# Performance work log

Hardware: AMD Instinct MI355X
Metric: run time of the kernel (lower is better)

## Reference

```python
import jax, jax.numpy as jnp
import numpy as np

CLIP = 50.0
EPS = 1e-8


def _attn_jacobian_agg(q, k, v, scale):
    """Aggregate attention Jacobian dO/dq summed over queries, plus attention outputs.

    q: (B, Q, d); k, v: (B, S, d).
    Per-query Jacobian: J_q = scale * sum_j p_j v_j (k_j - kbar)^T, kbar = sum_i p_i k_i.
    Returns (agg_jac: (B, d, d), outputs: (B, Q, d)).
    """
    scores = jnp.einsum('bqd,bsd->bqs', q, k) * scale
    p = jax.nn.softmax(scores, axis=-1)
    out = jnp.einsum('bqs,bsd->bqd', p, v)           # attention outputs O
    kbar = jnp.einsum('bqs,bsd->bqd', p, k)          # expected key per query
    # sum_j p_j v_j k_j^T  -> (B, Q, d, d)
    pvk = jnp.einsum('bqs,bsd,bse->bqde', p, v, k)
    jac = scale * (pvk - out[..., :, None] * kbar[..., None, :])
    return jac.sum(axis=1), out


def setup_inputs() -> dict:
    key = jax.random.key(0)
    ks = jax.random.split(key, 5)
    B, Q, S, M, D = 256, 16, 512, 8, 128
    return {
        'queries': jax.random.normal(ks[0], (B, Q, D), dtype=jnp.float32),
        'keys':    jax.random.normal(ks[1], (B, S, D), dtype=jnp.float32),
        'values':  jax.random.normal(ks[2], (B, S, D), dtype=jnp.float32),
        'k_cg':    jax.random.normal(ks[3], (B, M, D), dtype=jnp.float32),
        'v_cg':    jax.random.normal(ks[4], (B, M, D), dtype=jnp.float32),
    }


def reference(queries, keys, values, k_cg, v_cg):
    B, Q, d = queries.shape
    scale = d ** -0.5

    dense_jac, dense_out = _attn_jacobian_agg(queries, keys, values, scale)
    cg_jac, cg_out = _attn_jacobian_agg(queries, k_cg, v_cg, scale)

    # jacobian_clip_value = 50.0 (config default)
    dense_jac = jnp.clip(dense_jac, -CLIP, CLIP)
    cg_jac = jnp.clip(cg_jac, -CLIP, CLIP)

    df = dense_jac.reshape(B, -1)
    cf = cg_jac.reshape(B, -1)
    dn = jnp.linalg.norm(df, axis=-1)
    cn = jnp.linalg.norm(cf, axis=-1)
    cosine_sim = (df * cf).sum(axis=-1) / (dn * cn + EPS)
    force_direction_loss = 1.0 - cosine_sim

    # consistency: per-query output MSE, averaged over queries, scaled by 1/d_head
    out_diff = dense_out - cg_out
    per_query_mse = (out_diff ** 2).sum(axis=-1)          # (B, Q)
    consistency_loss = per_query_mse.sum(axis=-1) / Q / d  # (B,)

    # v4 loss: L = w_dir * L_force_cos + w_cons * L_consistency (defaults 1.0, 1.0)
    total = 1.0 * force_direction_loss + 1.0 * consistency_loss
    return total.mean()  # reduction='mean'
```

## Files before the change

### kernel.cpp

```cpp
#include <hip/hip_runtime.h>
#include <math.h>


namespace {
constexpr int Bn = 256, Qn = 16, Sn = 512, Mn = 8, Dn = 128;
constexpr int NT = 512;
constexpr float SCALE = 0.08838834764831845f;
constexpr float CLIPV = 50.0f;

constexpr int QS    = 0;
constexpr int PB    = 4352;
constexpr int WOFF  = 20992;
constexpr int ARENA = 23040;
constexpr int KT    = ARENA;
constexpr int VT    = ARENA + 18432;
constexpr int VTW   = ARENA + 27648;
constexpr int SCF   = ARENA;
constexpr int CGS   = 59904;
constexpr int PCG   = 60416;
constexpr int WC    = 61696;
constexpr int RED   = 61728;
constexpr int LDSZ  = 61856;

typedef __attribute__((ext_vector_type(8))) short bf16x8;
typedef __attribute__((ext_vector_type(4))) float f32x4;
#define MFMA16(a, b, c) __builtin_amdgcn_mfma_f32_16x16x32_bf16((a), (b), (c), 0, 0, 0)

__device__ inline unsigned int pack2t(float a, float b) {
  return __builtin_amdgcn_perm(__builtin_bit_cast(unsigned int, b),
                               __builtin_bit_cast(unsigned int, a), 0x07060302u);
}
__device__ inline unsigned short f2bf(float x) {
  unsigned int u = __builtin_bit_cast(unsigned int, x);
  u += 0x7fffu + ((u >> 16) & 1u);
  return (unsigned short)(u >> 16);
}
__device__ inline float bf2f(unsigned short h) {
  unsigned int u = ((unsigned int)h) << 16;
  return __builtin_bit_cast(float, u);
}
union Frag {
  bf16x8 v;
  unsigned int u[4];
  unsigned short h[8];
};

__global__ void zero_ws_kernel(float4* ws) {
  ws[threadIdx.x] = make_float4(0.f, 0.f, 0.f, 0.f);
}

__global__ void finalize_kernel(const float* __restrict__ ws, float* __restrict__ out) {
  __shared__ float sr[256];
  int i = threadIdx.x;
  float dt = ws[i * 4 + 0], n1 = ws[i * 4 + 1], n2 = ws[i * 4 + 2], cs = ws[i * 4 + 3];
  float cosv = dt / (sqrtf(n1) * sqrtf(n2) + 1e-8f);
  sr[i] = (1.0f - cosv) + cs * (1.0f / (float)(Qn * Dn));
  __syncthreads();
  for (int off = 128; off; off >>= 1) {
    if (i < off) sr[i] += sr[i + off];
    __syncthreads();
  }
  if (i == 0) out[0] = sr[0] * (1.0f / (float)Bn);
}

__global__ __launch_bounds__(NT, 4) void fm_kernel(
    const float* __restrict__ Qg, const float* __restrict__ Kg,
    const float* __restrict__ Vg, const float* __restrict__ Kcg,
    const float* __restrict__ Vcg, float* __restrict__ ws) {
  __shared__ __align__(16) char L[LDSZ];
  const int bid = blockIdx.x, b = bid >> 1, h = bid & 1;
  const int t = threadIdx.x, lane = t & 63, wv = t >> 6;
  const int quad = lane >> 4, l16 = lane & 15;

  const float* Qb = Qg + (size_t)b * Qn * Dn;
  const float* Kb = Kg + (size_t)b * Sn * Dn;
  const float* Vb = Vg + (size_t)b * Sn * Dn;
  const float* Kc = Kcg + (size_t)b * Mn * Dn;
  const float* Vc = Vcg + (size_t)b * Mn * Dn;

  const int dK = t & 127, gK = t >> 7;
  const int dV = t & 63, gV = t >> 6;
  float kpf[2][8], vpf[8];

  auto load_tiles = [&](int st) {
#pragma unroll
    for (int o = 0; o < 2; ++o) {
      int s0 = st * 64 + (gK + 4 * o) * 8;
#pragma unroll
      for (int i = 0; i < 8; ++i) kpf[o][i] = Kb[(size_t)(s0 + i) * Dn + dK];
    }
    int s1 = st * 64 + gV * 8;
#pragma unroll
    for (int i = 0; i < 8; ++i) vpf[i] = Vb[(size_t)(s1 + i) * Dn + h * 64 + dV];
  };
  auto store_tiles = [&](int st) {
#pragma unroll
    for (int o = 0; o < 2; ++o) {
      unsigned int u0 = pack2t(kpf[o][0], kpf[o][1]), u1 = pack2t(kpf[o][2], kpf[o][3]);
      unsigned int u2 = pack2t(kpf[o][4], kpf[o][5]), u3 = pack2t(kpf[o][6], kpf[o][7]);
      *(uint4*)(L + KT + dK * 144 + (gK + 4 * o) * 16) = make_uint4(u0, u1, u2, u3);
    }
    int s1 = st * 64 + gV * 8;
    float wv8[8];
#pragma unroll
    for (int i = 0; i < 8; ++i) wv8[i] = *(const float*)(L + WOFF + (s1 + i) * 4);
    unsigned int v0 = pack2t(vpf[0], vpf[1]), v1 = pack2t(vpf[2], vpf[3]);
    unsigned int v2 = pack2t(vpf[4], vpf[5]), v3 = pack2t(vpf[6], vpf[7]);
    *(uint4*)(L + VT + dV * 144 + gV * 16) = make_uint4(v0, v1, v2, v3);
    unsigned int w0 = pack2t(wv8[0] * vpf[0], wv8[1] * vpf[1]);
    unsigned int w1 = pack2t(wv8[2] * vpf[2], wv8[3] * vpf[3]);
    unsigned int w2 = pack2t(wv8[4] * vpf[4], wv8[5] * vpf[5]);
    unsigned int w3 = pack2t(wv8[6] * vpf[6], wv8[7] * vpf[7]);
    *(uint4*)(L + VTW + dV * 144 + gV * 16) = make_uint4(w0, w1, w2, w3);
  };

  {
    int row = t >> 5, c4 = t & 31;
    float4 qv = ((const float4*)Qb)[t];
    unsigned int p0 = pack2t(qv.x * SCALE, qv.y * SCALE);
    unsigned int p1 = pack2t(qv.z * SCALE, qv.w * SCALE);
    *(unsigned long long*)(L + QS + row * 272 + c4 * 8) =
        (unsigned long long)p0 | ((unsigned long long)p1 << 32);
  }
  load_tiles(0);
  __syncthreads();

  {
    bf16x8 aq[4];
#pragma unroll
    for (int kk = 0; kk < 4; ++kk)
      aq[kk] = *(const bf16x8*)(L + QS + l16 * 272 + kk * 64 + quad * 16);
    for (int j = 0; j < 4; ++j) {
      int srow = 64 * wv + 16 * j + l16;
      const float* kp = Kb + (size_t)srow * Dn + quad * 8;
      f32x4 acc = {0.f, 0.f, 0.f, 0.f};
#pragma unroll
      for (int kk = 0; kk < 4; ++kk) {
        float4 lo = *(const float4*)(kp + kk * 32);
        float4 hi = *(const float4*)(kp + kk * 32 + 4);
        Frag f;
        f.u[0] = pack2t(lo.x, lo.y);
        f.u[1] = pack2t(lo.z, lo.w);
        f.u[2] = pack2t(hi.x, hi.y);
        f.u[3] = pack2t(hi.z, hi.w);
        acc = MFMA16(aq[kk], f.v, acc);
      }
      int s = 64 * wv + 16 * j + l16;
#pragma unroll
      for (int r = 0; r < 4; ++r)
        *(float*)(L + SCF + (quad * 4 + r) * 2064 + s * 4) = acc[r];
    }
  }
  __syncthreads();

#pragma unroll
  for (int rr = 0; rr < 2; ++rr) {
    int q = wv * 2 + rr;
    const float* srow = (const float*)(L + SCF + q * 2064);
    float x[8];
    float m = -1e30f;
#pragma unroll
    for (int i = 0; i < 8; ++i) { x[i] = srow[lane * 8 + i]; m = fmaxf(m, x[i]); }
#pragma unroll
    for (int o = 32; o; o >>= 1) m = fmaxf(m, __shfl_xor(m, o));
    float ssum = 0.f;
#pragma unroll
    for (int i = 0; i < 8; ++i) { x[i] = __expf(x[i] - m); ssum += x[i]; }
#pragma unroll
    for (int o = 32; o; o >>= 1) ssum += __shfl_xor(ssum, o);
    float inv = 1.f / ssum;
    Frag g;
#pragma unroll
    for (int i = 0; i < 8; ++i) g.h[i] = f2bf(x[i] * inv);
    *(bf16x8*)(L + PB + q * 1040 + lane * 16) = g.v;
  }
  __syncthreads();
  {
    float wsv = 0.f;
#pragma unroll
    for (int q = 0; q < Qn; ++q)
      wsv += bf2f(*(const unsigned short*)(L + PB + q * 1040 + t * 2));
    *(float*)(L + WOFF + t * 4) = wsv;
  }
  __syncthreads();

  const int rp = wv & 1, ch = wv >> 1;
  f32x4 C00 = {0.f,0.f,0.f,0.f}, C01 = {0.f,0.f,0.f,0.f};
  f32x4 C10 = {0.f,0.f,0.f,0.f}, C11 = {0.f,0.f,0.f,0.f};
  f32x4 outacc = {0.f,0.f,0.f,0.f}, kbacc = {0.f,0.f,0.f,0.f};

  auto ckstep = [&](int colByte, f32x4& c00, f32x4& c01, f32x4& c10, f32x4& c11) {
    bf16x8 A0 = *(const bf16x8*)(L + VTW + (rp * 32 + l16) * 144 + colByte + quad * 16);
    bf16x8 A1 = *(const bf16x8*)(L + VTW + (rp * 32 + 16 + l16) * 144 + colByte + quad * 16);
    bf16x8 B0 = *(const bf16x8*)(L + KT + (ch * 32 + l16) * 144 + colByte + quad * 16);
    bf16x8 B1 = *(const bf16x8*)(L + KT + (ch * 32 + 16 + l16) * 144 + colByte + quad * 16);
    c00 = MFMA16(A0, B0, c00);
    c01 = MFMA16(A0, B1, c01);
    c10 = MFMA16(A1, B0, c10);
    c11 = MFMA16(A1, B1, c11);
  };

  for (int st = 0; st < 8; ++st) {
    if (st) __syncthreads();
    store_tiles(st);
    __syncthreads();
    if (st < 7) load_tiles(st + 1);
#pragma unroll
    for (int z = 0; z < 2; ++z) {
      int colByte = z * 64;
      bf16x8 pA = *(const bf16x8*)(L + PB + l16 * 1040 + st * 128 + z * 64 + quad * 16);
      bf16x8 bK = *(const bf16x8*)(L + KT + (wv * 16 + l16) * 144 + colByte + quad * 16);
      kbacc = MFMA16(pA, bK, kbacc);
      if (wv < 4) {
        bf16x8 bV = *(const bf16x8*)(L + VT + (wv * 16 + l16) * 144 + colByte + quad * 16);
        outacc = MFMA16(pA, bV, outacc);
      }
      ckstep(colByte, C00, C01, C10, C11);
    }
  }
  __syncthreads();

  if (wv < 4) {
#pragma unroll
    for (int r = 0; r < 4; ++r)
      *(unsigned short*)(L + VTW + (wv * 16 + l16) * 144 + (quad * 4 + r) * 2) = f2bf(-outacc[r]);
  }
#pragma unroll
  for (int r = 0; r < 4; ++r)
    *(unsigned short*)(L + KT + (wv * 16 + l16) * 144 + (quad * 4 + r) * 2) = f2bf(kbacc[r]);
  if (t < 256) {
    *(uint4*)(L + KT + (t >> 1) * 144 + 32 + (t & 1) * 16) = make_uint4(0, 0, 0, 0);
  } else if (t < 384) {
    int i = t - 256;
    *(uint4*)(L + VTW + (i >> 1) * 144 + 32 + (i & 1) * 16) = make_uint4(0, 0, 0, 0);
  }
  __syncthreads();
  ckstep(0, C00, C01, C10, C11);
#pragma unroll
  for (int r = 0; r < 4; ++r) {
    C00[r] = fminf(fmaxf(SCALE * C00[r], -CLIPV), CLIPV);
    C01[r] = fminf(fmaxf(SCALE * C01[r], -CLIPV), CLIPV);
    C10[r] = fminf(fmaxf(SCALE * C10[r], -CLIPV), CLIPV);
    C11[r] = fminf(fmaxf(SCALE * C11[r], -CLIPV), CLIPV);
  }
  __syncthreads();

  if (wv == 0) {
    f32x4 acc = {0.f, 0.f, 0.f, 0.f};
    const float* kp = Kc + (size_t)(l16 & 7) * Dn + quad * 8;
#pragma unroll
    for (int kk = 0; kk < 4; ++kk) {
      bf16x8 a = *(const bf16x8*)(L + QS + l16 * 272 + kk * 64 + quad * 16);
      float4 lo = *(const float4*)(kp + kk * 32);
      float4 hi = *(const float4*)(kp + kk * 32 + 4);
      Frag f;
      f.u[0] = pack2t(lo.x, lo.y);
      f.u[1] = pack2t(lo.z, lo.w);
      f.u[2] = pack2t(hi.x, hi.y);
      f.u[3] = pack2t(hi.z, hi.w);
      acc = MFMA16(a, f.v, acc);
    }
    if (l16 < 8) {
#pragma unroll
      for (int r = 0; r < 4; ++r)
        *(float*)(L + CGS + (quad * 4 + r) * 32 + l16 * 4) = acc[r];
    }
  }
  __syncthreads();
  if (t < 16) {
    float xs[8];
    float m = -1e30f;
#pragma unroll
    for (int s = 0; s < 8; ++s) { xs[s] = *(const float*)(L + CGS + t * 32 + s * 4); m = fmaxf(m, xs[s]); }
    float ssum = 0.f;
#pragma unroll
    for (int s = 0; s < 8; ++s) { xs[s] = __expf(xs[s] - m); ssum += xs[s]; }
    float inv = 1.f / ssum;
#pragma unroll
    for (int s = 0; s < 4; ++s)
      *(unsigned int*)(L + PCG + t * 80 + s * 4) = pack2t(xs[2 * s] * inv, xs[2 * s + 1] * inv);
#pragma unroll
    for (int p = 4; p < 16; ++p) *(unsigned int*)(L + PCG + t * 80 + p * 4) = 0u;
  }
  __syncthreads();
  if (t < 8) {
    float s = 0.f;
#pragma unroll
    for (int q = 0; q < Qn; ++q) s += bf2f(*(const unsigned short*)(L + PCG + q * 80 + t * 2));
    *(float*)(L + WC + t * 4) = s;
  }
  __syncthreads();
  if (t < 128) {
    float kv[8];
#pragma unroll
    for (int i = 0; i < 8; ++i) kv[i] = Kc[(size_t)i * Dn + t];
    *(uint4*)(L + KT + t * 144) = make_uint4(pack2t(kv[0], kv[1]), pack2t(kv[2], kv[3]),
                                             pack2t(kv[4], kv[5]), pack2t(kv[6], kv[7]));
    *(uint4*)(L + KT + t * 144 + 16) = make_uint4(0, 0, 0, 0);
    *(uint4*)(L + KT + t * 144 + 32) = make_uint4(0, 0, 0, 0);
    *(uint4*)(L + KT + t * 144 + 48) = make_uint4(0, 0, 0, 0);
  } else if (t < 192) {
    int d = t - 128;
    float vv2[8];
#pragma unroll
    for (int i = 0; i < 8; ++i) vv2[i] = Vc[(size_t)i * Dn + h * 64 + d];
    *(uint4*)(L + VT + d * 144) = make_uint4(pack2t(vv2[0], vv2[1]), pack2t(vv2[2], vv2[3]),
                                             pack2t(vv2[4], vv2[5]), pack2t(vv2[6], vv2[7]));
    *(uint4*)(L + VT + d * 144 + 16) = make_uint4(0, 0, 0, 0);
    *(uint4*)(L + VT + d * 144 + 32) = make_uint4(0, 0, 0, 0);
    *(uint4*)(L + VT + d * 144 + 48) = make_uint4(0, 0, 0, 0);
  } else if (t < 256) {
    int d = t - 192;
    float vv2[8], wcv[8];
#pragma unroll
    for (int i = 0; i < 8; ++i) {
      vv2[i] = Vc[(size_t)i * Dn + h * 64 + d];
      wcv[i] = *(const float*)(L + WC + i * 4);
    }
    *(uint4*)(L + VTW + d * 144) =
        make_uint4(pack2t(wcv[0] * vv2[0], wcv[1] * vv2[1]), pack2t(wcv[2] * vv2[2], wcv[3] * vv2[3]),
                   pack2t(wcv[4] * vv2[4], wcv[5] * vv2[5]), pack2t(wcv[6] * vv2[6], wcv[7] * vv2[7]));
    *(uint4*)(L + VTW + d * 144 + 16) = make_uint4(0, 0, 0, 0);
    *(uint4*)(L + VTW + d * 144 + 32) = make_uint4(0, 0, 0, 0);
    *(uint4*)(L + VTW + d * 144 + 48) = make_uint4(0, 0, 0, 0);
  }
  __syncthreads();
  f32x4 outc = {0.f,0.f,0.f,0.f}, kbc = {0.f,0.f,0.f,0.f};
  f32x4 D00 = {0.f,0.f,0.f,0.f}, D01 = {0.f,0.f,0.f,0.f};
  f32x4 D10 = {0.f,0.f,0.f,0.f}, D11 = {0.f,0.f,0.f,0.f};
  {
    bf16x8 pA = *(const bf16x8*)(L + PCG + l16 * 80 + quad * 16);
    bf16x8 bK = *(const bf16x8*)(L + KT + (wv * 16 + l16) * 144 + quad * 16);
    kbc = MFMA16(pA, bK, kbc);
    if (wv < 4) {
      bf16x8 bV = *(const bf16x8*)(L + VT + (wv * 16 + l16) * 144 + quad * 16);
      outc = MFMA16(pA, bV, outc);
    }
    ckstep(0, D00, D01, D10, D11);
  }
  __syncthreads();
  if (wv < 4) {
#pragma unroll
    for (int r = 0; r < 4; ++r)
      *(unsigned short*)(L + VTW + (wv * 16 + l16) * 144 + (quad * 4 + r) * 2) = f2bf(-outc[r]);
  }
#pragma unroll
  for (int r = 0; r < 4; ++r)
    *(unsigned short*)(L + KT + (wv * 16 + l16) * 144 + (quad * 4 + r) * 2) = f2bf(kbc[r]);
  __syncthreads();
  ckstep(0, D00, D01, D10, D11);
#pragma unroll
  for (int r = 0; r < 4; ++r) {
    D00[r] = fminf(fmaxf(SCALE * D00[r], -CLIPV), CLIPV);
    D01[r] = fminf(fmaxf(SCALE * D01[r], -CLIPV), CLIPV);
    D10[r] = fminf(fmaxf(SCALE * D10[r], -CLIPV), CLIPV);
    D11[r] = fminf(fmaxf(SCALE * D11[r], -CLIPV), CLIPV);
  }

  float dot = 0.f, nd2 = 0.f, nc2 = 0.f, cons = 0.f;
#pragma unroll
  for (int r = 0; r < 4; ++r) {
    dot += C00[r] * D00[r] + C01[r] * D01[r] + C10[r] * D10[r] + C11[r] * D11[r];
    nd2 += C00[r] * C00[r] + C01[r] * C01[r] + C10[r] * C10[r] + C11[r] * C11[r];
    nc2 += D00[r] * D00[r] + D01[r] * D01[r] + D10[r] * D10[r] + D11[r] * D11[r];
  }
  if (wv < 4) {
#pragma unroll
    for (int r = 0; r < 4; ++r) {
      float df = outacc[r] - outc[r];
      cons += df * df;
    }
  }
#pragma unroll
  for (int o = 32; o; o >>= 1) {
    dot += __shfl_xor(dot, o);
    nd2 += __shfl_xor(nd2, o);
    nc2 += __shfl_xor(nc2, o);
    cons += __shfl_xor(cons, o);
  }
  if (lane == 0) {
    float* red = (float*)(L + RED);
    red[wv * 4 + 0] = dot;
    red[wv * 4 + 1] = nd2;
    red[wv * 4 + 2] = nc2;
    red[wv * 4 + 3] = cons;
  }
  __syncthreads();
  if (t == 0) {
    const float* red = (const float*)(L + RED);
    float d_ = 0.f, n1 = 0.f, n2 = 0.f, cs = 0.f;
#pragma unroll
    for (int w = 0; w < 8; ++w) {
      d_ += red[w * 4 + 0];
      n1 += red[w * 4 + 1];
      n2 += red[w * 4 + 2];
      cs += red[w * 4 + 3];
    }
    atomicAdd(ws + b * 4 + 0, d_);
    atomicAdd(ws + b * 4 + 1, n1);
    atomicAdd(ws + b * 4 + 2, n2);
    atomicAdd(ws + b * 4 + 3, cs);
  }
}
}

extern "C" void kernel_launch(void* const* d_in, const int* in_sizes, int n_in,
                              void* d_out, int out_size, void* d_ws, size_t ws_size,
                              hipStream_t stream) {
  const float* q = (const float*)d_in[0];
  const float* k = (const float*)d_in[1];
  const float* v = (const float*)d_in[2];
  const float* kc = (const float*)d_in[3];
  const float* vc = (const float*)d_in[4];
  float* out = (float*)d_out;
  float* ws = (float*)d_ws;
  zero_ws_kernel<<<1, 256, 0, stream>>>((float4*)ws);
  fm_kernel<<<2 * Bn, NT, 0, stream>>>(q, k, v, kc, vc, ws);
  finalize_kernel<<<1, 256, 0, stream>>>(ws, out);
}
```

Measured before the change: 169.0 us.

## Double-buffer K/V register prefetch two stages ahead and prefetch cg tensors early

The K/V register prefetch becomes two buffers that load tiles two stages ahead, so global loads overlap more compute, and the first extra tile load is issued before the softmax. The small cg K/V loads are hoisted into stage 6 of the main loop to hide their latency. Blocks are remapped so the two halves of a batch sit 256 blocks apart, and the weight reads in store_tiles are vectorised into float4 loads. The extra register buffers raise VGPR pressure, which could hurt occupancy under launch_bounds(512,4) or cause spills.

```diff
diff --git a/kernel.cpp b/kernel.cpp
--- a/kernel.cpp
+++ b/kernel.cpp
@@ -68,7 +68,7 @@
     const float* __restrict__ Vg, const float* __restrict__ Kcg,
     const float* __restrict__ Vcg, float* __restrict__ ws) {
   __shared__ __align__(16) char L[LDSZ];
-  const int bid = blockIdx.x, b = bid >> 1, h = bid & 1;
+  const int bid = blockIdx.x, b = bid & 255, h = bid >> 8;
   const int t = threadIdx.x, lane = t & 63, wv = t >> 6;
   const int quad = lane >> 4, l16 = lane & 15;
 
@@ -80,9 +80,11 @@
 
   const int dK = t & 127, gK = t >> 7;
   const int dV = t & 63, gV = t >> 6;
-  float kpf[2][8], vpf[8];
-
-  auto load_tiles = [&](int st) {
+  float kpfA[2][8], vpfA[8];
+  float kpfB[2][8], vpfB[8];
+  float cgkv[8];
+
+  auto load_tiles = [&](int st, float (&kpf)[2][8], float (&vpf)[8]) {
 #pragma unroll
     for (int o = 0; o < 2; ++o) {
       int s0 = st * 64 + (gK + 4 * o) * 8;
@@ -93,7 +95,7 @@
 #pragma unroll
     for (int i = 0; i < 8; ++i) vpf[i] = Vb[(size_t)(s1 + i) * Dn + h * 64 + dV];
   };
-  auto store_tiles = [&](int st) {
+  auto store_tiles = [&](int st, float (&kpf)[2][8], float (&vpf)[8]) {
 #pragma unroll
     for (int o = 0; o < 2; ++o) {
       unsigned int u0 = pack2t(kpf[o][0], kpf[o][1]), u1 = pack2t(kpf[o][2], kpf[o][3]);
@@ -101,9 +103,9 @@
       *(uint4*)(L + KT + dK * 144 + (gK + 4 * o) * 16) = make_uint4(u0, u1, u2, u3);
     }
     int s1 = st * 64 + gV * 8;
-    float wv8[8];
-#pragma unroll
-    for (int i = 0; i < 8; ++i) wv8[i] = *(const float*)(L + WOFF + (s1 + i) * 4);
+    float4 wlo = *(const float4*)(L + WOFF + s1 * 4);
+    float4 whi = *(const float4*)(L + WOFF + s1 * 4 + 16);
+    float wv8[8] = {wlo.x, wlo.y, wlo.z, wlo.w, whi.x, whi.y, whi.z, whi.w};
     unsigned int v0 = pack2t(vpf[0], vpf[1]), v1 = pack2t(vpf[2], vpf[3]);
     unsigned int v2 = pack2t(vpf[4], vpf[5]), v3 = pack2t(vpf[6], vpf[7]);
     *(uint4*)(L + VT + dV * 144 + gV * 16) = make_uint4(v0, v1, v2, v3);
@@ -122,7 +124,7 @@
     *(unsigned long long*)(L + QS + row * 272 + c4 * 8) =
         (unsigned long long)p0 | ((unsigned long long)p1 << 32);
   }
-  load_tiles(0);
+  load_tiles(0, kpfA, vpfA);
   __syncthreads();
 
   {
@@ -151,6 +153,7 @@
         *(float*)(L + SCF + (quad * 4 + r) * 2064 + s * 4) = acc[r];
     }
   }
+  load_tiles(1, kpfB, vpfB);
   __syncthreads();
 
 #pragma unroll
@@ -200,11 +203,25 @@
     c11 = MFMA16(A1, B1, c11);
   };
 
+#pragma unroll 2
   for (int st = 0; st < 8; ++st) {
     if (st) __syncthreads();
-    store_tiles(st);
+    if (st & 1) store_tiles(st, kpfB, vpfB);
+    else       store_tiles(st, kpfA, vpfA);
     __syncthreads();
-    if (st < 7) load_tiles(st + 1);
+    if (st < 6) {
+      if (st & 1) load_tiles(st + 2, kpfB, vpfB);
+      else        load_tiles(st + 2, kpfA, vpfA);
+    } else if (st == 6) {
+      if (t < 128) {
+#pragma unroll
+        for (int i = 0; i < 8; ++i) cgkv[i] = Kc[(size_t)i * Dn + t];
+      } else if (t < 256) {
+        int d = (t - 128) & 63;
+#pragma unroll
+        for (int i = 0; i < 8; ++i) cgkv[i] = Vc[(size_t)i * Dn + h * 64 + d];
+      }
+    }
 #pragma unroll
     for (int z = 0; z < 2; ++z) {
       int colByte = z * 64;
@@ -291,35 +308,26 @@
   }
   __syncthreads();
   if (t < 128) {
-    float kv[8];
-#pragma unroll
-    for (int i = 0; i < 8; ++i) kv[i] = Kc[(size_t)i * Dn + t];
-    *(uint4*)(L + KT + t * 144) = make_uint4(pack2t(kv[0], kv[1]), pack2t(kv[2], kv[3]),
-                                             pack2t(kv[4], kv[5]), pack2t(kv[6], kv[7]));
+    *(uint4*)(L + KT + t * 144) = make_uint4(pack2t(cgkv[0], cgkv[1]), pack2t(cgkv[2], cgkv[3]),
+                                             pack2t(cgkv[4], cgkv[5]), pack2t(cgkv[6], cgkv[7]));
     *(uint4*)(L + KT + t * 144 + 16) = make_uint4(0, 0, 0, 0);
     *(uint4*)(L + KT + t * 144 + 32) = make_uint4(0, 0, 0, 0);
     *(uint4*)(L + KT + t * 144 + 48) = make_uint4(0, 0, 0, 0);
   } else if (t < 192) {
     int d = t - 128;
-    float vv2[8];
-#pragma unroll
-    for (int i = 0; i < 8; ++i) vv2[i] = Vc[(size_t)i * Dn + h * 64 + d];
-    *(uint4*)(L + VT + d * 144) = make_uint4(pack2t(vv2[0], vv2[1]), pack2t(vv2[2], vv2[3]),
-                                             pack2t(vv2[4], vv2[5]), pack2t(vv2[6], vv2[7]));
+    *(uint4*)(L + VT + d * 144) = make_uint4(pack2t(cgkv[0], cgkv[1]), pack2t(cgkv[2], cgkv[3]),
+                                             pack2t(cgkv[4], cgkv[5]), pack2t(cgkv[6], cgkv[7]));
     *(uint4*)(L + VT + d * 144 + 16) = make_uint4(0, 0, 0, 0);
     *(uint4*)(L + VT + d * 144 + 32) = make_uint4(0, 0, 0, 0);
     *(uint4*)(L + VT + d * 144 + 48) = make_uint4(0, 0, 0, 0);
   } else if (t < 256) {
     int d = t - 192;
-    float vv2[8], wcv[8];
-#pragma unroll
-    for (int i = 0; i < 8; ++i) {
-      vv2[i] = Vc[(size_t)i * Dn + h * 64 + d];
-      wcv[i] = *(const float*)(L + WC + i * 4);
-    }
+    float wcv[8];
+#pragma unroll
+    for (int i = 0; i < 8; ++i) wcv[i] = *(const float*)(L + WC + i * 4);
     *(uint4*)(L + VTW + d * 144) =
-        make_uint4(pack2t(wcv[0] * vv2[0], wcv[1] * vv2[1]), pack2t(wcv[2] * vv2[2], wcv[3] * vv2[3]),
-                   pack2t(wcv[4] * vv2[4], wcv[5] * vv2[5]), pack2t(wcv[6] * vv2[6], wcv[7] * vv2[7]));
+        make_uint4(pack2t(wcv[0] * cgkv[0], wcv[1] * cgkv[1]), pack2t(wcv[2] * cgkv[2], wcv[3] * cgkv[3]),
+                   pack2t(wcv[4] * cgkv[4], wcv[5] * cgkv[5]), pack2t(wcv[6] * cgkv[6], wcv[7] * cgkv[7]));
     *(uint4*)(L + VTW + d * 144 + 16) = make_uint4(0, 0, 0, 0);
     *(uint4*)(L + VTW + d * 144 + 32) = make_uint4(0, 0, 0, 0);
     *(uint4*)(L + VTW + d * 144 + 48) = make_uint4(0, 0, 0, 0);
```

Result: no change. 170.7 us (+1.0%).
